# Kernel tuning notes

Hardware: AMD Instinct MI355X
Metric: run time of the kernel (lower is better)

Reference implementation:

```python
import jax, jax.numpy as jnp
import numpy as np

N_TOTAL = 2_000_000
B = 50_000
D_MODEL = 128
HIDDEN = 64


def setup_inputs() -> dict:
    key = jax.random.key(0)
    ks = jax.random.split(key, 5)
    h = jax.random.normal(ks[0], (N_TOTAL, D_MODEL), dtype=jnp.float32)
    segment_ids = jnp.sort(jax.random.randint(ks[1], (N_TOTAL,), 0, B, dtype=jnp.int32))
    # MLP params (Linear stores [out,in] in torch; we use [in,out] with x @ W)
    W1 = jax.random.normal(ks[2], (D_MODEL, HIDDEN), dtype=jnp.float32) * (1.0 / np.sqrt(D_MODEL))
    b1 = jnp.zeros((HIDDEN,), dtype=jnp.float32)
    W2 = jax.random.normal(ks[3], (HIDDEN, HIDDEN), dtype=jnp.float32) * (1.0 / np.sqrt(HIDDEN))
    b2 = jnp.zeros((HIDDEN,), dtype=jnp.float32)
    W3 = jax.random.normal(ks[4], (HIDDEN, 1), dtype=jnp.float32) * (1.0 / np.sqrt(HIDDEN))
    b3 = jnp.zeros((1,), dtype=jnp.float32)
    return {"h": h, "segment_ids": segment_ids, "num_segments": B,
            "W1": W1, "b1": b1, "W2": W2, "b2": b2, "W3": W3, "b3": b3}


def reference(h, segment_ids, num_segments, W1, b1, W2, b2, W3, b3):
    # Ragged mean pooling over atoms -> [B, d_model] (fused segment reduce)
    sums = jax.ops.segment_sum(h, segment_ids, num_segments=num_segments)
    counts = jax.ops.segment_sum(jnp.ones((h.shape[0],), h.dtype), segment_ids,
                                 num_segments=num_segments)
    pooled = sums / jnp.maximum(counts, 1.0)[:, None]  # [B, d_model]
    # 3-layer MLP with SiLU -> scalar per molecule
    x = jax.nn.silu(pooled @ W1 + b1)
    x = jax.nn.silu(x @ W2 + b2)
    scalar = (x @ W3 + b3)[:, 0]  # [B]
    return scalar
```

## Files before the change

### kernel.cpp

```cpp
#include <hip/hip_runtime.h>

#define D_MODEL 128
#define HIDDEN 64
#define WPB 8
#define NTHREADS (WPB * 64)
#define NBLOCKS 512
#define W1_STRIDE 132
#define W2_STRIDE 68
#define SEG_BATCH 4

__global__ void seg_bounds_kernel(const int* __restrict__ seg, int n, int B,
                                  int* __restrict__ seg_start) {
  int i = blockIdx.x * blockDim.x + threadIdx.x;
  if (i >= n) return;
  int s = seg[i];
  if (i == 0) {
    for (int t = 0; t <= s; ++t) seg_start[t] = 0;
  } else {
    int p = seg[i - 1];
    for (int t = p + 1; t <= s; ++t) seg_start[t] = i;
  }
  if (i == n - 1) {
    for (int t = s + 1; t <= B; ++t) seg_start[t] = n;
  }
}

__device__ __forceinline__ float silu(float x) {
  return x / (1.0f + __expf(-x));
}
__device__ __forceinline__ float4 f4add(float4 a, float4 b) {
  return make_float4(a.x + b.x, a.y + b.y, a.z + b.z, a.w + b.w);
}
__device__ __forceinline__ float wave_sum(float p) {
#pragma unroll
  for (int off = 32; off >= 1; off >>= 1) p += __shfl_xor(p, off);
  return p;
}
__device__ __forceinline__ int lower_bound_ge(const int* __restrict__ arr,
                                              int B, int target) {
  int lo = 0, hi = B;
  while (lo < hi) {
    int m = (lo + hi) >> 1;
    if (arr[m] >= target) hi = m; else lo = m + 1;
  }
  return lo;
}

__global__ __launch_bounds__(NTHREADS, 4) void pool_mlp_kernel(
    const float* __restrict__ h, const int* __restrict__ seg_start,
    const float* __restrict__ W1, const float* __restrict__ b1,
    const float* __restrict__ W2, const float* __restrict__ b2,
    const float* __restrict__ W3, const float* __restrict__ b3,
    float* __restrict__ out, int B, int n_atoms) {
  __shared__ float sW1T[HIDDEN * W1_STRIDE];
  __shared__ float sW2T[HIDDEN * W2_STRIDE];
  __shared__ float pooled_lds[WPB][SEG_BATCH][D_MODEL];
  __shared__ float x1_lds[WPB][SEG_BATCH][HIDDEN];

  const int tid = threadIdx.x;

#pragma unroll
  for (int i = tid; i < (D_MODEL * HIDDEN) / 4; i += NTHREADS) {
    float4 v = reinterpret_cast<const float4*>(W1)[i];
    int k = i >> 4;
    int j = (4 * i) & (HIDDEN - 1);
    sW1T[(j + 0) * W1_STRIDE + k] = v.x;
    sW1T[(j + 1) * W1_STRIDE + k] = v.y;
    sW1T[(j + 2) * W1_STRIDE + k] = v.z;
    sW1T[(j + 3) * W1_STRIDE + k] = v.w;
  }
#pragma unroll
  for (int i = tid; i < (HIDDEN * HIDDEN) / 4; i += NTHREADS) {
    float4 v = reinterpret_cast<const float4*>(W2)[i];
    int k = i >> 4;
    int j = (4 * i) & (HIDDEN - 1);
    sW2T[(j + 0) * W2_STRIDE + k] = v.x;
    sW2T[(j + 1) * W2_STRIDE + k] = v.y;
    sW2T[(j + 2) * W2_STRIDE + k] = v.z;
    sW2T[(j + 3) * W2_STRIDE + k] = v.w;
  }

  const int wave = tid >> 6;
  const int lane = tid & 63;

  const int G = gridDim.x * WPB;
  const int g = blockIdx.x * WPB + wave;
  const int lo = (int)(((long long)g * n_atoms) / G);
  const int hi = (int)(((long long)(g + 1) * n_atoms) / G);
  const int my_s0 = lower_bound_ge(seg_start, B, lo);
  int s_end = (g == G - 1) ? B : lower_bound_ge(seg_start, B, hi);
  const int my_cnt = s_end - my_s0;

  __syncthreads();
  if (my_cnt <= 0) return;

  const float b1l = b1[lane];
  const float b2l = b2[lane];
  const float w3l = W3[lane];
  const float b3l = b3[0];

  const int half = lane >> 5;
  const int l32 = lane & 31;
  const float4* __restrict__ hv = reinterpret_cast<const float4*>(h);
  const float4* __restrict__ w1v =
      reinterpret_cast<const float4*>(&sW1T[lane * W1_STRIDE]);
  const float4* __restrict__ w2v =
      reinterpret_cast<const float4*>(&sW2T[lane * W2_STRIDE]);

  int start = seg_start[my_s0];
  for (int si = 0; si < my_cnt; si += SEG_BATCH) {
    const int nb = min(SEG_BATCH, my_cnt - si);

    int ends[SEG_BATCH];
#pragma unroll
    for (int b = 0; b < SEG_BATCH; ++b) {
      ends[b] = seg_start[my_s0 + si + min(b, nb - 1) + 1];
    }

    for (int b = 0; b < nb; ++b) {
      const int end = ends[b];
      const int cnt = end - start;
      float4 acc0 = make_float4(0.f, 0.f, 0.f, 0.f);
      float4 acc1 = acc0, acc2 = acc0, acc3 = acc0;
      int a = start + half;
      for (; a + 14 < end; a += 16) {
        float4 v0 = hv[(a + 0) * 32 + l32];
        float4 v1 = hv[(a + 2) * 32 + l32];
        float4 v2 = hv[(a + 4) * 32 + l32];
        float4 v3 = hv[(a + 6) * 32 + l32];
        float4 v4 = hv[(a + 8) * 32 + l32];
        float4 v5 = hv[(a + 10) * 32 + l32];
        float4 v6 = hv[(a + 12) * 32 + l32];
        float4 v7 = hv[(a + 14) * 32 + l32];
        acc0 = f4add(acc0, v0); acc1 = f4add(acc1, v1);
        acc2 = f4add(acc2, v2); acc3 = f4add(acc3, v3);
        acc0 = f4add(acc0, v4); acc1 = f4add(acc1, v5);
        acc2 = f4add(acc2, v6); acc3 = f4add(acc3, v7);
      }
      if (a + 6 < end) {
        float4 v0 = hv[(a + 0) * 32 + l32];
        float4 v1 = hv[(a + 2) * 32 + l32];
        float4 v2 = hv[(a + 4) * 32 + l32];
        float4 v3 = hv[(a + 6) * 32 + l32];
        acc0 = f4add(acc0, v0); acc1 = f4add(acc1, v1);
        acc2 = f4add(acc2, v2); acc3 = f4add(acc3, v3);
        a += 8;
      }
      if (a < end) {
        const int c1 = min(a + 2, n_atoms - 1);
        const int c2 = min(a + 4, n_atoms - 1);
        float4 v0 = hv[a * 32 + l32];
        float4 v1 = hv[c1 * 32 + l32];
        float4 v2 = hv[c2 * 32 + l32];
        acc0 = f4add(acc0, v0);
        if (a + 2 < end) acc1 = f4add(acc1, v1);
        if (a + 4 < end) acc2 = f4add(acc2, v2);
      }
      acc0 = f4add(f4add(acc0, acc1), f4add(acc2, acc3));
      acc0.x += __shfl_xor(acc0.x, 32);
      acc0.y += __shfl_xor(acc0.y, 32);
      acc0.z += __shfl_xor(acc0.z, 32);
      acc0.w += __shfl_xor(acc0.w, 32);
      const float inv = 1.0f / (float)max(cnt, 1);
      if (half == 0) {
        reinterpret_cast<float4*>(&pooled_lds[wave][b][0])[l32] = make_float4(
            acc0.x * inv, acc0.y * inv, acc0.z * inv, acc0.w * inv);
      }
      start = end;
    }
    __builtin_amdgcn_wave_barrier();

    const float4* pv0 = reinterpret_cast<const float4*>(&pooled_lds[wave][0][0]);
    const float4* pv1 = reinterpret_cast<const float4*>(&pooled_lds[wave][1][0]);
    const float4* pv2 = reinterpret_cast<const float4*>(&pooled_lds[wave][2][0]);
    const float4* pv3 = reinterpret_cast<const float4*>(&pooled_lds[wave][3][0]);
    float a1b0 = b1l, a1b1 = b1l, a1b2 = b1l, a1b3 = b1l;
#pragma unroll 8
    for (int t = 0; t < D_MODEL / 4; ++t) {
      float4 w = w1v[t];
      float4 p0 = pv0[t], p1 = pv1[t], p2 = pv2[t], p3 = pv3[t];
      a1b0 = fmaf(p0.x, w.x, a1b0); a1b0 = fmaf(p0.y, w.y, a1b0);
      a1b0 = fmaf(p0.z, w.z, a1b0); a1b0 = fmaf(p0.w, w.w, a1b0);
      a1b1 = fmaf(p1.x, w.x, a1b1); a1b1 = fmaf(p1.y, w.y, a1b1);
      a1b1 = fmaf(p1.z, w.z, a1b1); a1b1 = fmaf(p1.w, w.w, a1b1);
      a1b2 = fmaf(p2.x, w.x, a1b2); a1b2 = fmaf(p2.y, w.y, a1b2);
      a1b2 = fmaf(p2.z, w.z, a1b2); a1b2 = fmaf(p2.w, w.w, a1b2);
      a1b3 = fmaf(p3.x, w.x, a1b3); a1b3 = fmaf(p3.y, w.y, a1b3);
      a1b3 = fmaf(p3.z, w.z, a1b3); a1b3 = fmaf(p3.w, w.w, a1b3);
    }
    x1_lds[wave][0][lane] = silu(a1b0);
    x1_lds[wave][1][lane] = silu(a1b1);
    x1_lds[wave][2][lane] = silu(a1b2);
    x1_lds[wave][3][lane] = silu(a1b3);
    __builtin_amdgcn_wave_barrier();

    const float4* x10 = reinterpret_cast<const float4*>(&x1_lds[wave][0][0]);
    const float4* x11 = reinterpret_cast<const float4*>(&x1_lds[wave][1][0]);
    const float4* x12 = reinterpret_cast<const float4*>(&x1_lds[wave][2][0]);
    const float4* x13 = reinterpret_cast<const float4*>(&x1_lds[wave][3][0]);
    float a2b0 = b2l, a2b1 = b2l, a2b2 = b2l, a2b3 = b2l;
#pragma unroll 8
    for (int t = 0; t < HIDDEN / 4; ++t) {
      float4 w = w2v[t];
      float4 p0 = x10[t], p1 = x11[t], p2 = x12[t], p3 = x13[t];
      a2b0 = fmaf(p0.x, w.x, a2b0); a2b0 = fmaf(p0.y, w.y, a2b0);
      a2b0 = fmaf(p0.z, w.z, a2b0); a2b0 = fmaf(p0.w, w.w, a2b0);
      a2b1 = fmaf(p1.x, w.x, a2b1); a2b1 = fmaf(p1.y, w.y, a2b1);
      a2b1 = fmaf(p1.z, w.z, a2b1); a2b1 = fmaf(p1.w, w.w, a2b1);
      a2b2 = fmaf(p2.x, w.x, a2b2); a2b2 = fmaf(p2.y, w.y, a2b2);
      a2b2 = fmaf(p2.z, w.z, a2b2); a2b2 = fmaf(p2.w, w.w, a2b2);
      a2b3 = fmaf(p3.x, w.x, a2b3); a2b3 = fmaf(p3.y, w.y, a2b3);
      a2b3 = fmaf(p3.z, w.z, a2b3); a2b3 = fmaf(p3.w, w.w, a2b3);
    }
    float r0 = wave_sum(silu(a2b0) * w3l);
    float r1 = wave_sum(silu(a2b1) * w3l);
    float r2 = wave_sum(silu(a2b2) * w3l);
    float r3 = wave_sum(silu(a2b3) * w3l);
    float val = (lane == 0) ? r0 : (lane == 1) ? r1 : (lane == 2) ? r2 : r3;
    if (lane < nb) out[my_s0 + si + lane] = val + b3l;
  }
}

extern "C" void kernel_launch(void* const* d_in, const int* in_sizes, int n_in,
                              void* d_out, int out_size, void* d_ws, size_t ws_size,
                              hipStream_t stream) {
  const float* h = (const float*)d_in[0];
  const int* seg = (const int*)d_in[1];
  const float* W1 = (const float*)d_in[3];
  const float* b1 = (const float*)d_in[4];
  const float* W2 = (const float*)d_in[5];
  const float* b2 = (const float*)d_in[6];
  const float* W3 = (const float*)d_in[7];
  const float* b3 = (const float*)d_in[8];
  float* out = (float*)d_out;

  const int n = in_sizes[1];
  const int B = out_size;

  int* seg_start = (int*)d_ws;

  {
    int threads = 256;
    int blocks = (n + threads - 1) / threads;
    seg_bounds_kernel<<<blocks, threads, 0, stream>>>(seg, n, B, seg_start);
  }
  {
    pool_mlp_kernel<<<NBLOCKS, NTHREADS, 0, stream>>>(
        h, seg_start, W1, b1, W2, b2, W3, b3, out, B, n);
  }
}
```

Baseline: 206.4 us.

## Split fused pool+MLP kernel into separate pooling and MLP kernels

Splits the fused segment-mean-pooling and MLP kernel into two launches. A lightweight pool kernel with more blocks and smaller blocks streams h and writes pooled vectors to workspace, and a separate MLP kernel reads them back in batches of four. The pooling kernel no longer pays for the LDS weight staging and its occupancy limits, so it can keep more memory traffic in flight. The cost is an extra kernel launch plus a write and re-read of a B×128 pooled buffer in global memory, and the pooling inner loop is less unrolled.

```diff
diff --git a/kernel.cpp b/kernel.cpp
--- a/kernel.cpp
+++ b/kernel.cpp
@@ -2,9 +2,14 @@
 
 #define D_MODEL 128
 #define HIDDEN 64
-#define WPB 8
-#define NTHREADS (WPB * 64)
-#define NBLOCKS 512
+
+#define P_WPB 4
+#define P_NTHREADS 256
+#define P_NBLOCKS 2048
+
+#define M_WPB 8
+#define M_NTHREADS 512
+#define M_NBLOCKS 512
 #define W1_STRIDE 132
 #define W2_STRIDE 68
 #define SEG_BATCH 4
@@ -46,21 +51,69 @@
   return lo;
 }
 
-__global__ __launch_bounds__(NTHREADS, 4) void pool_mlp_kernel(
+__global__ __launch_bounds__(P_NTHREADS, 8) void pool_kernel(
     const float* __restrict__ h, const int* __restrict__ seg_start,
+    float* __restrict__ pooled, int B, int n_atoms) {
+  const int wave = threadIdx.x >> 6;
+  const int lane = threadIdx.x & 63;
+  const int G = gridDim.x * P_WPB;
+  const int g = blockIdx.x * P_WPB + wave;
+  const int lo = (int)(((long long)g * n_atoms) / G);
+  const int hi = (int)(((long long)(g + 1) * n_atoms) / G);
+  const int my_s0 = lower_bound_ge(seg_start, B, lo);
+  const int s_end = (g == G - 1) ? B : lower_bound_ge(seg_start, B, hi);
+  if (s_end <= my_s0) return;
+
+  const int half = lane >> 5;
+  const int l32 = lane & 31;
+  const float4* __restrict__ hv = reinterpret_cast<const float4*>(h);
+  float4* __restrict__ pooledv = reinterpret_cast<float4*>(pooled);
+
+  int start = seg_start[my_s0];
+  for (int s = my_s0; s < s_end; ++s) {
+    const int end = seg_start[s + 1];
+    const int cnt = end - start;
+    float4 acc0 = make_float4(0.f, 0.f, 0.f, 0.f);
+    float4 acc1 = acc0;
+    int a = start + half;
+    for (; a + 2 < end; a += 4) {
+      float4 v0 = hv[a * 32 + l32];
+      float4 v1 = hv[(a + 2) * 32 + l32];
+      acc0 = f4add(acc0, v0);
+      acc1 = f4add(acc1, v1);
+    }
+    if (a < end) {
+      float4 v0 = hv[a * 32 + l32];
+      acc0 = f4add(acc0, v0);
+    }
+    acc0 = f4add(acc0, acc1);
+    acc0.x += __shfl_xor(acc0.x, 32);
+    acc0.y += __shfl_xor(acc0.y, 32);
+    acc0.z += __shfl_xor(acc0.z, 32);
+    acc0.w += __shfl_xor(acc0.w, 32);
+    const float inv = 1.0f / (float)max(cnt, 1);
+    if (half == 0) {
+      pooledv[s * 32 + l32] = make_float4(acc0.x * inv, acc0.y * inv,
+                                          acc0.z * inv, acc0.w * inv);
+    }
+    start = end;
+  }
+}
+
+__global__ __launch_bounds__(M_NTHREADS, 4) void mlp_kernel(
+    const float* __restrict__ pooled,
     const float* __restrict__ W1, const float* __restrict__ b1,
     const float* __restrict__ W2, const float* __restrict__ b2,
     const float* __restrict__ W3, const float* __restrict__ b3,
-    float* __restrict__ out, int B, int n_atoms) {
+    float* __restrict__ out, int B) {
   __shared__ float sW1T[HIDDEN * W1_STRIDE];
   __shared__ float sW2T[HIDDEN * W2_STRIDE];
-  __shared__ float pooled_lds[WPB][SEG_BATCH][D_MODEL];
-  __shared__ float x1_lds[WPB][SEG_BATCH][HIDDEN];
+  __shared__ float pooled_lds[M_WPB][SEG_BATCH][D_MODEL];
+  __shared__ float x1_lds[M_WPB][SEG_BATCH][HIDDEN];
 
   const int tid = threadIdx.x;
-
-#pragma unroll
-  for (int i = tid; i < (D_MODEL * HIDDEN) / 4; i += NTHREADS) {
+#pragma unroll
+  for (int i = tid; i < (D_MODEL * HIDDEN) / 4; i += M_NTHREADS) {
     float4 v = reinterpret_cast<const float4*>(W1)[i];
     int k = i >> 4;
     int j = (4 * i) & (HIDDEN - 1);
@@ -70,7 +123,7 @@
     sW1T[(j + 3) * W1_STRIDE + k] = v.w;
   }
 #pragma unroll
-  for (int i = tid; i < (HIDDEN * HIDDEN) / 4; i += NTHREADS) {
+  for (int i = tid; i < (HIDDEN * HIDDEN) / 4; i += M_NTHREADS) {
     float4 v = reinterpret_cast<const float4*>(W2)[i];
     int k = i >> 4;
     int j = (4 * i) & (HIDDEN - 1);
@@ -79,94 +132,35 @@
     sW2T[(j + 2) * W2_STRIDE + k] = v.z;
     sW2T[(j + 3) * W2_STRIDE + k] = v.w;
   }
+  __syncthreads();
 
   const int wave = tid >> 6;
   const int lane = tid & 63;
-
-  const int G = gridDim.x * WPB;
-  const int g = blockIdx.x * WPB + wave;
-  const int lo = (int)(((long long)g * n_atoms) / G);
-  const int hi = (int)(((long long)(g + 1) * n_atoms) / G);
-  const int my_s0 = lower_bound_ge(seg_start, B, lo);
-  int s_end = (g == G - 1) ? B : lower_bound_ge(seg_start, B, hi);
-  const int my_cnt = s_end - my_s0;
-
-  __syncthreads();
-  if (my_cnt <= 0) return;
-
+  const int half = lane >> 5;
+  const int l32 = lane & 31;
   const float b1l = b1[lane];
   const float b2l = b2[lane];
   const float w3l = W3[lane];
   const float b3l = b3[0];
 
-  const int half = lane >> 5;
-  const int l32 = lane & 31;
-  const float4* __restrict__ hv = reinterpret_cast<const float4*>(h);
+  const float4* __restrict__ pooledv = reinterpret_cast<const float4*>(pooled);
   const float4* __restrict__ w1v =
       reinterpret_cast<const float4*>(&sW1T[lane * W1_STRIDE]);
   const float4* __restrict__ w2v =
       reinterpret_cast<const float4*>(&sW2T[lane * W2_STRIDE]);
 
-  int start = seg_start[my_s0];
-  for (int si = 0; si < my_cnt; si += SEG_BATCH) {
-    const int nb = min(SEG_BATCH, my_cnt - si);
-
-    int ends[SEG_BATCH];
-#pragma unroll
-    for (int b = 0; b < SEG_BATCH; ++b) {
-      ends[b] = seg_start[my_s0 + si + min(b, nb - 1) + 1];
-    }
-
-    for (int b = 0; b < nb; ++b) {
-      const int end = ends[b];
-      const int cnt = end - start;
-      float4 acc0 = make_float4(0.f, 0.f, 0.f, 0.f);
-      float4 acc1 = acc0, acc2 = acc0, acc3 = acc0;
-      int a = start + half;
-      for (; a + 14 < end; a += 16) {
-        float4 v0 = hv[(a + 0) * 32 + l32];
-        float4 v1 = hv[(a + 2) * 32 + l32];
-        float4 v2 = hv[(a + 4) * 32 + l32];
-        float4 v3 = hv[(a + 6) * 32 + l32];
-        float4 v4 = hv[(a + 8) * 32 + l32];
-        float4 v5 = hv[(a + 10) * 32 + l32];
-        float4 v6 = hv[(a + 12) * 32 + l32];
-        float4 v7 = hv[(a + 14) * 32 + l32];
-        acc0 = f4add(acc0, v0); acc1 = f4add(acc1, v1);
-        acc2 = f4add(acc2, v2); acc3 = f4add(acc3, v3);
-        acc0 = f4add(acc0, v4); acc1 = f4add(acc1, v5);
-        acc2 = f4add(acc2, v6); acc3 = f4add(acc3, v7);
-      }
-      if (a + 6 < end) {
-        float4 v0 = hv[(a + 0) * 32 + l32];
-        float4 v1 = hv[(a + 2) * 32 + l32];
-        float4 v2 = hv[(a + 4) * 32 + l32];
-        float4 v3 = hv[(a + 6) * 32 + l32];
-        acc0 = f4add(acc0, v0); acc1 = f4add(acc1, v1);
-        acc2 = f4add(acc2, v2); acc3 = f4add(acc3, v3);
-        a += 8;
-      }
-      if (a < end) {
-        const int c1 = min(a + 2, n_atoms - 1);
-        const int c2 = min(a + 4, n_atoms - 1);
-        float4 v0 = hv[a * 32 + l32];
-        float4 v1 = hv[c1 * 32 + l32];
-        float4 v2 = hv[c2 * 32 + l32];
-        acc0 = f4add(acc0, v0);
-        if (a + 2 < end) acc1 = f4add(acc1, v1);
-        if (a + 4 < end) acc2 = f4add(acc2, v2);
-      }
-      acc0 = f4add(f4add(acc0, acc1), f4add(acc2, acc3));
-      acc0.x += __shfl_xor(acc0.x, 32);
-      acc0.y += __shfl_xor(acc0.y, 32);
-      acc0.z += __shfl_xor(acc0.z, 32);
-      acc0.w += __shfl_xor(acc0.w, 32);
-      const float inv = 1.0f / (float)max(cnt, 1);
-      if (half == 0) {
-        reinterpret_cast<float4*>(&pooled_lds[wave][b][0])[l32] = make_float4(
-            acc0.x * inv, acc0.y * inv, acc0.z * inv, acc0.w * inv);
-      }
-      start = end;
+  const int GW = gridDim.x * M_WPB;
+  const int nbatch = (B + SEG_BATCH - 1) / SEG_BATCH;
+  for (int batch = blockIdx.x * M_WPB + wave; batch < nbatch; batch += GW) {
+    const int s0 = batch * SEG_BATCH;
+    const int nb = min(SEG_BATCH, B - s0);
+
+#pragma unroll
+    for (int b = 0; b < SEG_BATCH; b += 2) {
+      const int bb = b + half;
+      const int sb = s0 + min(bb, nb - 1);
+      reinterpret_cast<float4*>(&pooled_lds[wave][bb][0])[l32] =
+          pooledv[sb * 32 + l32];
     }
     __builtin_amdgcn_wave_barrier();
 
@@ -217,7 +211,7 @@
     float r2 = wave_sum(silu(a2b2) * w3l);
     float r3 = wave_sum(silu(a2b3) * w3l);
     float val = (lane == 0) ? r0 : (lane == 1) ? r1 : (lane == 2) ? r2 : r3;
-    if (lane < nb) out[my_s0 + si + lane] = val + b3l;
+    if (lane < nb) out[s0 + lane] = val + b3l;
   }
 }
 
@@ -238,14 +232,15 @@
   const int B = out_size;
 
   int* seg_start = (int*)d_ws;
+  size_t pooled_off = ((size_t)(B + 1) * sizeof(int) + 255) & ~(size_t)255;
+  float* pooled = (float*)((char*)d_ws + pooled_off);
 
   {
     int threads = 256;
     int blocks = (n + threads - 1) / threads;
     seg_bounds_kernel<<<blocks, threads, 0, stream>>>(seg, n, B, seg_start);
   }
-  {
-    pool_mlp_kernel<<<NBLOCKS, NTHREADS, 0, stream>>>(
-        h, seg_start, W1, b1, W2, b2, W3, b3, out, B, n);
-  }
-}
+  pool_kernel<<<P_NBLOCKS, P_NTHREADS, 0, stream>>>(h, seg_start, pooled, B, n);
+  mlp_kernel<<<M_NBLOCKS, M_NTHREADS, 0, stream>>>(
+      pooled, W1, b1, W2, b2, W3, b3, out, B);
+}
```

After: 269.2 us. +30.5%, slower.
